# Kernel tuning notes

Measured on AMD Instinct MI355X. Metric: run time of the kernel, lower is better.

Reference implementation:

```python
import jax, jax.numpy as jnp
import numpy as np

H, INNER, V = 64, 32, 64
LR = 0.05
B, L = 256, 2048


def setup_inputs() -> dict:
    key = jax.random.key(0)
    ks = jax.random.split(key, 8)
    s = 0.05
    return {
        "seq":   jax.random.randint(ks[0], (B, L), 0, V),
        "embed": jax.random.normal(ks[1], (V, H), jnp.float32) * s,
        "ffw1":  jax.random.normal(ks[2], (2 * H, H), jnp.float32) * s,
        "ffb1":  jnp.zeros((2 * H,), jnp.float32),
        "ffw2":  jax.random.normal(ks[3], (H, 2 * H), jnp.float32) * s,
        "ffb2":  jnp.zeros((H,), jnp.float32),
        "ln_g":  jnp.ones((H,), jnp.float32),
        "ln_b":  jnp.zeros((H,), jnp.float32),
        "w1":    jax.random.normal(ks[4], (INNER, H), jnp.float32) * s,
        "b1":    jnp.zeros((INNER,), jnp.float32),
        "w2":    jax.random.normal(ks[5], (H, INNER), jnp.float32) * s,
        "b2":    jnp.zeros((H,), jnp.float32),
        "wout":  jax.random.normal(ks[6], (V, H), jnp.float32) * s,
        "bout":  jnp.zeros((V,), jnp.float32),
    }


def _encoder(seq, embed, ffw1, ffb1, ffw2, ffb2, ln_g, ln_b):
    e = embed[seq]                                             # [B,L,H]
    ff = jnp.maximum(e @ ffw1.T + ffb1, 0.0) @ ffw2.T + ffb2   # [B,L,H]
    x = e + ff
    mu = x.mean(-1, keepdims=True)
    var = x.var(-1, keepdims=True)                             # biased, like nn.LayerNorm
    return (x - mu) / jnp.sqrt(var + 1e-5) * ln_g + ln_b


def _ttt_one(kseq, vseq, last, w1, b1, w2, b2):
    # Sequential inner-loop TTT: per (k,v) pair, one SGD step on the tiny MLP
    # with analytic gradients of MSE(pred, v) (mean over H).
    def step(carry, kv):
        w1c, b1c, w2c, b2c = carry
        k, v = kv
        pre = w1c @ k + b1c                # [INNER]
        h = jnp.maximum(pre, 0.0)
        pred = w2c @ h + b2c               # [H]
        d = (2.0 / H) * (pred - v)         # dL/dpred
        gw2 = jnp.outer(d, h)
        gb2 = d
        dh = (w2c.T @ d) * (pre > 0.0)
        gw1 = jnp.outer(dh, k)
        gb1 = dh
        return (w1c - LR * gw1, b1c - LR * gb1,
                w2c - LR * gw2, b2c - LR * gb2), None

    (w1f, b1f, w2f, b2f), _ = jax.lax.scan(step, (w1, b1, w2, b2), (kseq, vseq))
    return w2f @ jnp.maximum(w1f @ last + b1f, 0.0) + b2f


def reference(seq, embed, ffw1, ffb1, ffw2, ffb2, ln_g, ln_b,
              w1, b1, w2, b2, wout, bout):
    hs = _encoder(seq, embed, ffw1, ffb1, ffw2, ffb2, ln_g, ln_b)
    hs = jax.lax.stop_gradient(hs)         # torch detaches kh/vh/last
    Lc = hs.shape[1]
    nsteps = (Lc - 2) // 2                 # len(range(0, L-3, 2))
    kseq = hs[:, 0:Lc - 3:2]               # [B,nsteps,H]
    vseq = hs[:, 1:Lc - 2:2][:, :nsteps]   # [B,nsteps,H]
    w1_0 = jax.lax.stop_gradient(w1)
    b1_0 = jax.lax.stop_gradient(b1)
    w2_0 = jax.lax.stop_gradient(w2)
    b2_0 = jax.lax.stop_gradient(b2)
    ctxs = jax.vmap(_ttt_one, in_axes=(0, 0, 0, None, None, None, None))(
        kseq, vseq, hs[:, -1], w1_0, b1_0, w2_0, b2_0)  # [B,H]
    return ctxs @ wout.T + bout            # [B,V]
```

## Files before the change

### kernel.cpp

```cpp
#include <hip/hip_runtime.h>

#define HD 64
#define VOCAB 64
#define BATCH 256
#define SEQLEN 2048
#define NSTEPS ((SEQLEN - 2) / 2)
#define LRc 0.05f

typedef __attribute__((ext_vector_type(2))) float f2;

__device__ __forceinline__ float xsum32(float x) {
  unsigned int u = __float_as_uint(x);
  auto r = __builtin_amdgcn_permlane32_swap(u, u, false, false);
  return __uint_as_float(r[0]) + __uint_as_float(r[1]);
}

__global__ __launch_bounds__(64, 1) void enc_build(
    const float* __restrict__ embed, const float* __restrict__ ffw1,
    const float* __restrict__ ffb1, const float* __restrict__ ffw2,
    const float* __restrict__ ffb2, const float* __restrict__ ln_g,
    const float* __restrict__ ln_b, float* __restrict__ enc) {
  const int v = blockIdx.x, j = threadIdx.x;
  __shared__ float e_s[HD];
  __shared__ float hid_s[2 * HD];
  float e = embed[v * HD + j];
  e_s[j] = e;
  __syncthreads();
  float ha = ffb1[j], hb = ffb1[HD + j];
  #pragma unroll 8
  for (int h = 0; h < HD; ++h) {
    float eh = e_s[h];
    ha = fmaf(ffw1[j * HD + h], eh, ha);
    hb = fmaf(ffw1[(HD + j) * HD + h], eh, hb);
  }
  hid_s[j] = fmaxf(ha, 0.f);
  hid_s[HD + j] = fmaxf(hb, 0.f);
  __syncthreads();
  float ff = ffb2[j];
  #pragma unroll 8
  for (int h2 = 0; h2 < 2 * HD; ++h2) ff = fmaf(ffw2[j * 2 * HD + h2], hid_s[h2], ff);
  float x = e + ff;
  float mu = x;
  #pragma unroll
  for (int m = 1; m < 64; m <<= 1) mu += __shfl_xor(mu, m, 64);
  mu *= (1.f / 64.f);
  float xc = x - mu;
  float var = xc * xc;
  #pragma unroll
  for (int m = 1; m < 64; m <<= 1) var += __shfl_xor(var, m, 64);
  var *= (1.f / 64.f);
  enc[v * HD + j] = xc / sqrtf(var + 1e-5f) * ln_g[j] + ln_b[j];
}

__global__ __launch_bounds__(64, 1) void gram_build(
    const float* __restrict__ enc, float* __restrict__ G) {
  __shared__ float es[VOCAB * HD];
  const int u = blockIdx.x, v = threadIdx.x;
  #pragma unroll
  for (int q = 0; q < 16; ++q)
    ((float4*)es)[v + 64 * q] = ((const float4*)enc)[v + 64 * q];
  __syncthreads();
  const float* a = &es[u * HD];
  const float* bb = &es[v * HD];
  float s0 = 0.f, s1 = 0.f, s2 = 0.f, s3 = 0.f;
  #pragma unroll
  for (int j = 0; j < HD; j += 4) {
    s0 = fmaf(a[j + 0], bb[j + 0], s0);
    s1 = fmaf(a[j + 1], bb[j + 1], s1);
    s2 = fmaf(a[j + 2], bb[j + 2], s2);
    s3 = fmaf(a[j + 3], bb[j + 3], s3);
  }
  G[u * VOCAB + v] = (s0 + s1) + (s2 + s3);
}

__device__ __forceinline__ void ttt_step(
    int l, int i, int half,
    const float* __restrict__ enc_s, const float* __restrict__ G_s,
    const int* __restrict__ seq_s, float* __restrict__ sd_s,
    float* __restrict__ h_s,
    f2 (&W1)[16], f2 (&W2R2)[16], f2 (&W2T)[16],
    float& b1r, float& b2r,
    f2 (&KC)[16], float& vvC, f2 (&KX)[16], float& vvN,
    f2 (&SD)[16], float& hp,
    float& POFb, float& KKF, float& dhp,
    int2& tk, int2& tk1, int pidx) {
  float pre = fmaf(dhp, KKF, POFb);
  float h = fmaxf(pre, 0.f);

  h_s[i] = h;
  f2 H2[16];
  {
    float4* h4 = (float4*)&H2[0];
    #pragma unroll
    for (int q = 0; q < 8; ++q) h4[q] = *(const float4*)&h_s[4 * q];
  }

  f2 dhp2 = {dhp, dhp};
  #pragma unroll
  for (int c = 0; c < 16; ++c) W1[c] = __builtin_elementwise_fma(dhp2, KX[c], W1[c]);

  const float* krn = &enc_s[tk1.x * HD + half * 32];
  float4* kx4 = (float4*)&KX[0];
  #pragma unroll
  for (int q = 0; q < 8; ++q) kx4[q] = *(const float4*)&krn[4 * q];
  vvN = enc_s[tk1.y * HD + l];
  float KKFn = G_s[tk.x * VOCAB + tk1.x];
  int2 tk2 = *(const int2*)&seq_s[pidx];

  f2 hp2 = {hp, hp};
  #pragma unroll
  for (int r = 0; r < 16; ++r) W2T[r] = __builtin_elementwise_fma(SD[r], hp2, W2T[r]);

  f2 qa = {b2r, 0.f}, qb = {0.f, 0.f}, qc = {0.f, 0.f}, qd = {0.f, 0.f};
  #pragma unroll
  for (int c = 0; c < 16; c += 4) {
    qa = __builtin_elementwise_fma(W2R2[c + 0], H2[c + 0], qa);
    qb = __builtin_elementwise_fma(W2R2[c + 1], H2[c + 1], qb);
    qc = __builtin_elementwise_fma(W2R2[c + 2], H2[c + 2], qc);
    qd = __builtin_elementwise_fma(W2R2[c + 3], H2[c + 3], qd);
  }
  f2 qs = (qa + qb) + (qc + qd);
  float pred = qs.x + qs.y;
  float sR = (vvC - pred) * (2.f * LRc / (float)HD);
  sd_s[l] = sR;

  {
    const float* drp = &sd_s[half * 32];
    float4* sd4 = (float4*)&SD[0];
    #pragma unroll
    for (int q = 0; q < 8; ++q) sd4[q] = *(const float4*)&drp[4 * q];
  }

  f2 sr2 = {sR, sR};
  #pragma unroll
  for (int c = 0; c < 16; ++c) W2R2[c] = __builtin_elementwise_fma(sr2, H2[c], W2R2[c]);
  b2r += sR;
  f2 p0 = {0.f, 0.f}, p1 = {0.f, 0.f};
  #pragma unroll
  for (int c = 0; c < 16; c += 2) {
    p0 = __builtin_elementwise_fma(W1[c + 0], KX[c + 0], p0);
    p1 = __builtin_elementwise_fma(W1[c + 1], KX[c + 1], p1);
  }
  f2 ps = p0 + p1;
  float PB = xsum32(ps.x + ps.y) + b1r;

  f2 g0 = {0.f, 0.f}, g1 = {0.f, 0.f};
  #pragma unroll
  for (int r = 0; r < 16; r += 2) {
    g0 = __builtin_elementwise_fma(W2T[r + 0], SD[r + 0], g0);
    g1 = __builtin_elementwise_fma(W2T[r + 1], SD[r + 1], g1);
  }
  f2 gs = g0 + g1;
  float dh = xsum32(gs.x + gs.y);
  dh = (pre > 0.f) ? dh : 0.f;

  b1r += dh;
  POFb = PB + dh;
  KKF = KKFn;
  dhp = dh;
  hp = h;
  tk = tk1;
  tk1 = tk2;
}

__global__ __launch_bounds__(64, 1) void ttt_run(
    const int* __restrict__ seq, const float* __restrict__ enc,
    const float* __restrict__ Gg,
    const float* __restrict__ w1g, const float* __restrict__ b1g,
    const float* __restrict__ w2g, const float* __restrict__ b2g,
    const float* __restrict__ woutg, const float* __restrict__ boutg,
    float* __restrict__ out) {
  __shared__ float enc_s[VOCAB * HD];
  __shared__ float G_s[VOCAB * VOCAB];
  __shared__ int   seq_s[SEQLEN];
  __shared__ float sd_s[64];
  __shared__ float h_s[32];
  __shared__ float ctx_s[64];
  const int b = blockIdx.x, l = threadIdx.x;
  const int i = l & 31, half = l >> 5;

  #pragma unroll
  for (int q = 0; q < 16; ++q)
    ((float4*)enc_s)[l + 64 * q] = ((const float4*)enc)[l + 64 * q];
  #pragma unroll
  for (int q = 0; q < 16; ++q)
    ((float4*)G_s)[l + 64 * q] = ((const float4*)Gg)[l + 64 * q];
  const int4* seqg = (const int4*)(seq + b * SEQLEN);
  #pragma unroll
  for (int q = 0; q < 8; ++q)
    ((int4*)seq_s)[l + 64 * q] = seqg[l + 64 * q];

  f2 W1[16], W2R2[16], W2T[16];
  {
    float4* w14 = (float4*)&W1[0];
    #pragma unroll
    for (int q = 0; q < 8; ++q) w14[q] = *(const float4*)&w1g[i * 64 + half * 32 + 4 * q];
    float4* w2r4 = (float4*)&W2R2[0];
    #pragma unroll
    for (int q = 0; q < 8; ++q) w2r4[q] = *(const float4*)&w2g[l * 32 + 4 * q];
  }
  #pragma unroll
  for (int r = 0; r < 16; ++r)
    W2T[r] = f2{w2g[(half * 32 + 2 * r) * 32 + i], w2g[(half * 32 + 2 * r + 1) * 32 + i]};
  float b1r = b1g[i];
  float b2r = b2g[l];
  __syncthreads();

  int2 tk  = *(const int2*)&seq_s[0];
  int2 tk1 = *(const int2*)&seq_s[2];
  f2 KA[16], KB[16], SD[16];
  float vvA, vvB;
  {
    const float* kr = &enc_s[tk.x * HD + half * 32];
    float4* ka4 = (float4*)&KA[0];
    #pragma unroll
    for (int q = 0; q < 8; ++q) ka4[q] = *(const float4*)&kr[4 * q];
    vvA = enc_s[tk.y * HD + l];
  }
  #pragma unroll
  for (int c = 0; c < 16; ++c) { KB[c] = f2{0.f, 0.f}; SD[c] = f2{0.f, 0.f}; }
  float hp = 0.f;

  float POFb, KKF = 0.f, dhp = 0.f;
  {
    f2 p0 = {0.f, 0.f}, p1 = {0.f, 0.f};
    #pragma unroll
    for (int c = 0; c < 16; c += 2) {
      p0 = __builtin_elementwise_fma(W1[c + 0], KA[c + 0], p0);
      p1 = __builtin_elementwise_fma(W1[c + 1], KA[c + 1], p1);
    }
    f2 ps = p0 + p1;
    POFb = xsum32(ps.x + ps.y) + b1r;
  }

  for (int s = 0; s < NSTEPS - 1; s += 2) {
    ttt_step(l, i, half, enc_s, G_s, seq_s, sd_s, h_s, W1, W2R2, W2T, b1r, b2r,
             KA, vvA, KB, vvB, SD, hp, POFb, KKF, dhp, tk, tk1, 2 * s + 4);
    ttt_step(l, i, half, enc_s, G_s, seq_s, sd_s, h_s, W1, W2R2, W2T, b1r, b2r,
             KB, vvB, KA, vvA, SD, hp, POFb, KKF, dhp, tk, tk1, 2 * s + 6);
  }
  ttt_step(l, i, half, enc_s, G_s, seq_s, sd_s, h_s, W1, W2R2, W2T, b1r, b2r,
           KA, vvA, KB, vvB, SD, hp, POFb, KKF, dhp, tk, tk1, 2046 );

  {
    f2 dhp2 = {dhp, dhp};
    #pragma unroll
    for (int c = 0; c < 16; ++c) W1[c] = __builtin_elementwise_fma(dhp2, KA[c], W1[c]);
  }

  {
    int tok = seq_s[SEQLEN - 1];
    f2 K[16];
    const float* kr = &enc_s[tok * HD + half * 32];
    float4* k4 = (float4*)&K[0];
    #pragma unroll
    for (int q = 0; q < 8; ++q) k4[q] = *(const float4*)&kr[4 * q];
    f2 a0 = {0.f, 0.f}, a1 = {0.f, 0.f};
    #pragma unroll
    for (int c = 0; c < 16; c += 2) {
      a0 = __builtin_elementwise_fma(W1[c + 0], K[c + 0], a0);
      a1 = __builtin_elementwise_fma(W1[c + 1], K[c + 1], a1);
    }
    f2 as = a0 + a1;
    float pre = xsum32(as.x + as.y) + b1r;
    float h = fmaxf(pre, 0.f);
    h_s[i] = h;
    f2 H2[16];
    {
      float4* h4 = (float4*)&H2[0];
      #pragma unroll
      for (int q = 0; q < 8; ++q) h4[q] = *(const float4*)&h_s[4 * q];
    }
    f2 qa = {b2r, 0.f}, qb = {0.f, 0.f}, qc = {0.f, 0.f}, qd = {0.f, 0.f};
    #pragma unroll
    for (int c = 0; c < 16; c += 4) {
      qa = __builtin_elementwise_fma(W2R2[c + 0], H2[c + 0], qa);
      qb = __builtin_elementwise_fma(W2R2[c + 1], H2[c + 1], qb);
      qc = __builtin_elementwise_fma(W2R2[c + 2], H2[c + 2], qc);
      qd = __builtin_elementwise_fma(W2R2[c + 3], H2[c + 3], qd);
    }
    f2 qs = (qa + qb) + (qc + qd);
    ctx_s[l] = qs.x + qs.y;
    __syncthreads();
    float acc = boutg[l];
    #pragma unroll 8
    for (int jj = 0; jj < 64; ++jj) acc = fmaf(woutg[l * 64 + jj], ctx_s[jj], acc);
    out[b * 64 + l] = acc;
  }
}

extern "C" void kernel_launch(void* const* d_in, const int* in_sizes, int n_in,
                              void* d_out, int out_size, void* d_ws, size_t ws_size,
                              hipStream_t stream) {
  const int*   seq   = (const int*)d_in[0];
  const float* embed = (const float*)d_in[1];
  const float* ffw1  = (const float*)d_in[2];
  const float* ffb1  = (const float*)d_in[3];
  const float* ffw2  = (const float*)d_in[4];
  const float* ffb2  = (const float*)d_in[5];
  const float* ln_g  = (const float*)d_in[6];
  const float* ln_b  = (const float*)d_in[7];
  const float* w1    = (const float*)d_in[8];
  const float* b1    = (const float*)d_in[9];
  const float* w2    = (const float*)d_in[10];
  const float* b2    = (const float*)d_in[11];
  const float* wout  = (const float*)d_in[12];
  const float* bout  = (const float*)d_in[13];
  float* enc = (float*)d_ws;
  float* G   = (float*)d_ws + 4096;

  enc_build<<<VOCAB, 64, 0, stream>>>(embed, ffw1, ffb1, ffw2, ffb2, ln_g, ln_b, enc);
  gram_build<<<VOCAB, 64, 0, stream>>>(enc, G);
  ttt_run<<<BATCH, 64, 0, stream>>>(seq, enc, G, w1, b1, w2, b2, wout, bout, (float*)d_out);
}
```

Before: 380.3 us.

## Triple-buffer key vectors to prefetch one step further ahead in TTT loop

Switches the sequential TTT scan from two rotating key register buffers to three, so the shared-memory load of the key two steps ahead is issued at the end of each step, after the dependent reductions. The loop is unrolled by three with clamped sequence indices, replacing the remainder step. This aims to hide LDS latency behind the serial per-step dependency chain, at the cost of 32 more VGPRs and some tail-index clamping.

```diff
diff --git a/kernel.cpp b/kernel.cpp
--- a/kernel.cpp
+++ b/kernel.cpp
@@ -80,14 +80,15 @@
     float* __restrict__ h_s,
     f2 (&W1)[16], f2 (&W2R2)[16], f2 (&W2T)[16],
     float& b1r, float& b2r,
-    f2 (&KC)[16], float& vvC, f2 (&KX)[16], float& vvN,
+    f2 (&Kdef)[16], f2 (&Kpof)[16],
+    float& vvC, float& vvN,
     f2 (&SD)[16], float& hp,
     float& POFb, float& KKF, float& dhp,
-    int2& tk, int2& tk1, int pidx) {
+    int2& tk, int2& tk1, int2& tk2, int pidx) {
   float pre = fmaf(dhp, KKF, POFb);
   float h = fmaxf(pre, 0.f);
-
   h_s[i] = h;
+
   f2 H2[16];
   {
     float4* h4 = (float4*)&H2[0];
@@ -97,15 +98,11 @@
 
   f2 dhp2 = {dhp, dhp};
   #pragma unroll
-  for (int c = 0; c < 16; ++c) W1[c] = __builtin_elementwise_fma(dhp2, KX[c], W1[c]);
-
-  const float* krn = &enc_s[tk1.x * HD + half * 32];
-  float4* kx4 = (float4*)&KX[0];
-  #pragma unroll
-  for (int q = 0; q < 8; ++q) kx4[q] = *(const float4*)&krn[4 * q];
+  for (int c = 0; c < 16; ++c) W1[c] = __builtin_elementwise_fma(dhp2, Kdef[c], W1[c]);
+
   vvN = enc_s[tk1.y * HD + l];
   float KKFn = G_s[tk.x * VOCAB + tk1.x];
-  int2 tk2 = *(const int2*)&seq_s[pidx];
+  int2 tk3 = *(const int2*)&seq_s[pidx];
 
   f2 hp2 = {hp, hp};
   #pragma unroll
@@ -138,8 +135,8 @@
   f2 p0 = {0.f, 0.f}, p1 = {0.f, 0.f};
   #pragma unroll
   for (int c = 0; c < 16; c += 2) {
-    p0 = __builtin_elementwise_fma(W1[c + 0], KX[c + 0], p0);
-    p1 = __builtin_elementwise_fma(W1[c + 1], KX[c + 1], p1);
+    p0 = __builtin_elementwise_fma(W1[c + 0], Kpof[c + 0], p0);
+    p1 = __builtin_elementwise_fma(W1[c + 1], Kpof[c + 1], p1);
   }
   f2 ps = p0 + p1;
   float PB = xsum32(ps.x + ps.y) + b1r;
@@ -153,6 +150,13 @@
   f2 gs = g0 + g1;
   float dh = xsum32(gs.x + gs.y);
   dh = (pre > 0.f) ? dh : 0.f;
+
+  {
+    const float* krn = &enc_s[tk2.x * HD + half * 32];
+    float4* k4 = (float4*)&Kdef[0];
+    #pragma unroll
+    for (int q = 0; q < 8; ++q) k4[q] = *(const float4*)&krn[4 * q];
+  }
 
   b1r += dh;
   POFb = PB + dh;
@@ -161,6 +165,7 @@
   hp = h;
   tk = tk1;
   tk1 = tk2;
+  tk2 = tk3;
 }
 
 __global__ __launch_bounds__(64, 1) void ttt_run(
@@ -208,17 +213,22 @@
 
   int2 tk  = *(const int2*)&seq_s[0];
   int2 tk1 = *(const int2*)&seq_s[2];
-  f2 KA[16], KB[16], SD[16];
-  float vvA, vvB;
-  {
-    const float* kr = &enc_s[tk.x * HD + half * 32];
-    float4* ka4 = (float4*)&KA[0];
-    #pragma unroll
-    for (int q = 0; q < 8; ++q) ka4[q] = *(const float4*)&kr[4 * q];
-    vvA = enc_s[tk.y * HD + l];
-  }
-  #pragma unroll
-  for (int c = 0; c < 16; ++c) { KB[c] = f2{0.f, 0.f}; SD[c] = f2{0.f, 0.f}; }
+  int2 tk2 = *(const int2*)&seq_s[4];
+  f2 K0[16], K1[16], K2[16], SD[16];
+  float vv0, vv1 = 0.f, vv2 = 0.f;
+  {
+    const float* kr1 = &enc_s[tk.x * HD + half * 32];
+    float4* k14 = (float4*)&K1[0];
+    #pragma unroll
+    for (int q = 0; q < 8; ++q) k14[q] = *(const float4*)&kr1[4 * q];
+    const float* kr2 = &enc_s[tk1.x * HD + half * 32];
+    float4* k24 = (float4*)&K2[0];
+    #pragma unroll
+    for (int q = 0; q < 8; ++q) k24[q] = *(const float4*)&kr2[4 * q];
+    vv0 = enc_s[tk.y * HD + l];
+  }
+  #pragma unroll
+  for (int c = 0; c < 16; ++c) { K0[c] = f2{0.f, 0.f}; SD[c] = f2{0.f, 0.f}; }
   float hp = 0.f;
 
   float POFb, KKF = 0.f, dhp = 0.f;
@@ -226,26 +236,29 @@
     f2 p0 = {0.f, 0.f}, p1 = {0.f, 0.f};
     #pragma unroll
     for (int c = 0; c < 16; c += 2) {
-      p0 = __builtin_elementwise_fma(W1[c + 0], KA[c + 0], p0);
-      p1 = __builtin_elementwise_fma(W1[c + 1], KA[c + 1], p1);
+      p0 = __builtin_elementwise_fma(W1[c + 0], K1[c + 0], p0);
+      p1 = __builtin_elementwise_fma(W1[c + 1], K1[c + 1], p1);
     }
     f2 ps = p0 + p1;
     POFb = xsum32(ps.x + ps.y) + b1r;
   }
 
-  for (int s = 0; s < NSTEPS - 1; s += 2) {
+  for (int s = 0; s < NSTEPS / 3; ++s) {
+    int p0i = 6 * s + 6;  if (p0i > 2046) p0i = 2046;
+    int p1i = 6 * s + 8;  if (p1i > 2046) p1i = 2046;
+    int p2i = 6 * s + 10; if (p2i > 2046) p2i = 2046;
     ttt_step(l, i, half, enc_s, G_s, seq_s, sd_s, h_s, W1, W2R2, W2T, b1r, b2r,
-             KA, vvA, KB, vvB, SD, hp, POFb, KKF, dhp, tk, tk1, 2 * s + 4);
+             K0, K2, vv0, vv1, SD, hp, POFb, KKF, dhp, tk, tk1, tk2, p0i);
     ttt_step(l, i, half, enc_s, G_s, seq_s, sd_s, h_s, W1, W2R2, W2T, b1r, b2r,
-             KB, vvB, KA, vvA, SD, hp, POFb, KKF, dhp, tk, tk1, 2 * s + 6);
-  }
-  ttt_step(l, i, half, enc_s, G_s, seq_s, sd_s, h_s, W1, W2R2, W2T, b1r, b2r,
-           KA, vvA, KB, vvB, SD, hp, POFb, KKF, dhp, tk, tk1, 2046 );
+             K1, K0, vv1, vv2, SD, hp, POFb, KKF, dhp, tk, tk1, tk2, p1i);
+    ttt_step(l, i, half, enc_s, G_s, seq_s, sd_s, h_s, W1, W2R2, W2T, b1r, b2r,
+             K2, K1, vv2, vv0, SD, hp, POFb, KKF, dhp, tk, tk1, tk2, p2i);
+  }
 
   {
     f2 dhp2 = {dhp, dhp};
     #pragma unroll
-    for (int c = 0; c < 16; ++c) W1[c] = __builtin_elementwise_fma(dhp2, KA[c], W1[c]);
+    for (int c = 0; c < 16; ++c) W1[c] = __builtin_elementwise_fma(dhp2, K0[c], W1[c]);
   }
 
   {
```

Result: slower. 444.8 us (+16.9%).
